# Optimization experiments

Measured on AMD Instinct MI355X. Metric: run time of the kernel, lower is better.

## Reference

```python
import jax, jax.numpy as jnp
import numpy as np
import math

B, L, D = 4, 2048, 1024        # batch, x_len, x_dim
QKV, H = 64, 16                # qkv_dim, head_dim (number of heads)


def setup_inputs() -> dict:
    key = jax.random.key(0)
    ks = jax.random.split(key, 10)
    s = 1.0 / math.sqrt(D)
    return {
        "x": jax.random.normal(ks[0], (B, L, D), jnp.float32),
        "encoder_x": jax.random.normal(ks[1], (B, L, D), jnp.float32),
        "Wq": jax.random.normal(ks[2], (D, QKV * H), jnp.float32) * s,
        "bq": jax.random.normal(ks[3], (QKV * H,), jnp.float32) * 0.01,
        "Wk": jax.random.normal(ks[4], (D, QKV * H), jnp.float32) * s,
        "bk": jax.random.normal(ks[5], (QKV * H,), jnp.float32) * 0.01,
        "Wv": jax.random.normal(ks[6], (D, QKV * H), jnp.float32) * s,
        "bv": jax.random.normal(ks[7], (QKV * H,), jnp.float32) * 0.01,
        "Wo": jax.random.normal(ks[8], (QKV * H, D), jnp.float32) * s,
        "bo": jax.random.normal(ks[9], (D,), jnp.float32) * 0.01,
    }


def reference(x, encoder_x, Wq, bq, Wk, bk, Wv, bv, Wo, bo):
    # q,k from encoder_x; v from x  -> [B, L, H, QKV]
    q = (encoder_x @ Wq + bq).reshape(B, L, H, QKV)
    k = (encoder_x @ Wk + bk).reshape(B, L, H, QKV)
    v = (x @ Wv + bv).reshape(B, L, H, QKV)
    # explicit [B,H,L,L] score matrix + softmax over k (faithful to source)
    scores = jax.nn.softmax(
        jnp.einsum("bqhd,bkhd->bhqk", q, k) / math.sqrt(QKV), axis=-1
    )
    # faithful to source einsum 'bvhd,bhqk->bvhd': no shared contraction
    # index, so scores are summed over (q,k) and broadcast onto v per (b,h).
    attn = jnp.einsum("bvhd,bhqk->bvhd", v, scores).reshape(B, L, H * QKV)
    return attn @ Wo + bo
```

## Files before the change

kernel.cpp:

```cpp
#include <hip/hip_runtime.h>
#include <stdint.h>


typedef __attribute__((ext_vector_type(8))) short bf16x8;
typedef __attribute__((ext_vector_type(4))) float f32x4;

typedef __attribute__((address_space(1))) void as1_void;
typedef __attribute__((address_space(3))) void as3_void;
#define GLD16(g, s)                                                          \
  __builtin_amdgcn_global_load_lds((as1_void*)(g), (as3_void*)(s), 16, 0, 0)

__device__ __forceinline__ short f2bf(float f) {
  union { float f; uint32_t u; } v; v.f = f;
  uint32_t r = v.u + 0x7FFFu + ((v.u >> 16) & 1u);
  return (short)(r >> 16);
}

__device__ __forceinline__ bf16x8 pack8(f32x4 a, f32x4 b) {
  union { f32x4 f; uint32_t u[4]; } x, y;
  x.f = a; y.f = b;
#pragma unroll
  for (int t = 0; t < 4; ++t) x.u[t] += 0x8000u;
#pragma unroll
  for (int t = 0; t < 4; ++t) y.u[t] += 0x8000u;
  union { bf16x8 v; uint32_t u[4]; } o;
  o.u[0] = __builtin_amdgcn_perm(x.u[1], x.u[0], 0x07060302);
  o.u[1] = __builtin_amdgcn_perm(x.u[3], x.u[2], 0x07060302);
  o.u[2] = __builtin_amdgcn_perm(y.u[1], y.u[0], 0x07060302);
  o.u[3] = __builtin_amdgcn_perm(y.u[3], y.u[2], 0x07060302);
  return o.v;
}

__global__ __launch_bounds__(256) void wgemm(
    const float* __restrict__ Wo, const float* __restrict__ Wv,
    const float* __restrict__ bv, const float* __restrict__ bo,
    short* __restrict__ Wt, float* __restrict__ biasc) {
  constexpr int BK = 64, NW = 1024;
  __shared__ __align__(16) float Bsf[64 * BK];
  __shared__ __align__(16) float Ts[64 * 36];
  const int b = blockIdx.x, tid = threadIdx.x;

  if (b >= 512) {
    float* red = Bsf;
    const int b3 = b - 512;
    const int nx = tid & 15, ky = tid >> 4;
    const int n = b3 * 16 + nx;
    float s = 0.f;
    for (int k = ky; k < 1024; k += 16)
      s += bv[k] * Wo[(size_t)k * NW + n];
    red[tid] = s;
    __syncthreads();
#pragma unroll
    for (int st = 128; st >= 16; st >>= 1) {
      if (tid < st) red[tid] += red[tid + st];
      __syncthreads();
    }
    if (ky == 0) biasc[n] = 2048.0f * red[nx] + bo[n];
    return;
  }

  const int lane = tid & 63, wave = tid >> 6;
  const int bm = (b >> 4) * 32, bn = (b & 15) * 64;
  const int wm = (wave & 1) * 16, wn = (wave >> 1) * 32;
  const int l15 = lane & 15, quad = lane >> 4;

  f32x4 acc[2];
  acc[0] = (f32x4){0.f, 0.f, 0.f, 0.f};
  acc[1] = (f32x4){0.f, 0.f, 0.f, 0.f};

  const int br = tid >> 4, bc4 = (tid & 15) ^ (br & 7);
  const float* pb = Wv + (size_t)(bn + br) * NW + bc4 * 4;
  float* lb = Bsf + tid * 4;

  const int ajr = tid >> 3, ac4 = (tid & 7) * 4;
  const float* pa = Wo + (size_t)ajr * NW + bm + ac4;

  for (int kt = 0; kt < 1024; kt += BK) {
    float4 va = *(const float4*)(pa);
    float4 vb = *(const float4*)(pa + 32 * (size_t)NW);
    pa += (size_t)BK * NW;
#pragma unroll
    for (int s = 0; s < 4; ++s) GLD16(pb + (size_t)(16 * s) * NW, lb + 1024 * s);
    pb += BK;
    *(float4*)(Ts + ajr * 36 + ac4) = va;
    *(float4*)(Ts + (ajr + 32) * 36 + ac4) = vb;
    __syncthreads();
#pragma unroll
    for (int kk = 0; kk < 2; ++kk) {
      const float* tsp = Ts + ((kk * 4 + quad) * 8) * 36 + wm + l15;
      float av[8];
#pragma unroll
      for (int e = 0; e < 8; ++e) av[e] = tsp[e * 36];
      bf16x8 af = pack8((f32x4){av[0], av[1], av[2], av[3]},
                        (f32x4){av[4], av[5], av[6], av[7]});
#pragma unroll
      for (int j = 0; j < 2; ++j) {
        const int rn = wn + j * 16 + l15;
        const int c4 = kk * 8 + quad * 2;
        f32x4 u0 = *(const f32x4*)(Bsf + (rn * 16 + (c4 ^ (rn & 7))) * 4);
        f32x4 u1 = *(const f32x4*)(Bsf + (rn * 16 + ((c4 + 1) ^ (rn & 7))) * 4);
        acc[j] = __builtin_amdgcn_mfma_f32_16x16x32_bf16(af, pack8(u0, u1),
                                                         acc[j], 0, 0, 0);
      }
    }
    __syncthreads();
  }
#pragma unroll
  for (int j = 0; j < 2; ++j) {
    const int col = bn + wn + j * 16 + l15;
    const int row0 = bm + wm + quad * 4;
#pragma unroll
    for (int r = 0; r < 4; ++r)
      Wt[(size_t)(row0 + r) * NW + col] = f2bf(2048.f * acc[j][r]);
  }
}

__global__ __launch_bounds__(256) void gemm_main(
    const float* __restrict__ X, const short* __restrict__ Bt,
    const float* __restrict__ bias, float* __restrict__ Out,
    int M, int N, int K) {
  constexpr int BK = 64;
  __shared__ __align__(16) char smem[65536];
  short* As0 = (short*)smem;
  short* As1 = (short*)(smem + 16384);
  short* Bs0 = (short*)(smem + 32768);
  short* Bs1 = (short*)(smem + 49152);
  const int tid = threadIdx.x, lane = tid & 63, wave = tid >> 6;
  const int b = blockIdx.x;
  const int bm = (b & 63) * 128;
  const int bn = (b >> 6) * 128;
  const int wm = (wave & 1) * 64, wn = (wave >> 1) * 64;
  const int l15 = lane & 15, quad = lane >> 4;

  f32x4 acc[4][4];
#pragma unroll
  for (int i = 0; i < 4; ++i)
#pragma unroll
    for (int j = 0; j < 4; ++j) acc[i][j] = (f32x4){0.f, 0.f, 0.f, 0.f};

  const int srow = tid >> 3, sc8 = (tid & 7) ^ (srow & 7);
  const float* pa = X + (size_t)(bm + srow) * K + sc8 * 8;
  const short* pb = Bt + (size_t)(bn + srow) * K + sc8 * 8;

  float4 a0[4], a1[4];

#define LOADA(kt)                                                            \
  {                                                                          \
    _Pragma("unroll") for (int s = 0; s < 4; ++s) {                          \
      const float* p = pa + (size_t)(32 * s) * K + (kt);                     \
      a0[s] = *(const float4*)(p);                                           \
      a1[s] = *(const float4*)(p + 4);                                       \
    }                                                                        \
  }
#define LOADB(Bsx, kt)                                                       \
  {                                                                          \
    _Pragma("unroll") for (int s = 0; s < 4; ++s)                            \
        GLD16(pb + (size_t)(32 * s) * K + (kt), (Bsx) + tid * 8 + 2048 * s); \
  }
#define PACKWRITE(Asx)                                                       \
  {                                                                          \
    _Pragma("unroll") for (int s = 0; s < 4; ++s)                            \
        *(bf16x8*)((Asx) + tid * 8 + 2048 * s) =                             \
            pack8((f32x4){a0[s].x, a0[s].y, a0[s].z, a0[s].w},               \
                  (f32x4){a1[s].x, a1[s].y, a1[s].z, a1[s].w});              \
  }
#define COMPUTE(Asx, Bsx)                                                    \
  {                                                                          \
    _Pragma("unroll") for (int kk = 0; kk < 2; ++kk) {                       \
      bf16x8 af[4], bfr[4];                                                  \
      _Pragma("unroll") for (int i = 0; i < 4; ++i) {                        \
        const int r = wm + i * 16 + l15;                                     \
        af[i] = *(const bf16x8*)((Asx) + r * BK +                            \
                                 ((kk * 4 + quad) ^ (r & 7)) * 8);           \
      }                                                                      \
      _Pragma("unroll") for (int j = 0; j < 4; ++j) {                        \
        const int r = wn + j * 16 + l15;                                     \
        bfr[j] = *(const bf16x8*)((Bsx) + r * BK +                           \
                                  ((kk * 4 + quad) ^ (r & 7)) * 8);          \
      }                                                                      \
      _Pragma("unroll") for (int i = 0; i < 4; ++i)                          \
          _Pragma("unroll") for (int j = 0; j < 4; ++j)                      \
              acc[i][j] = __builtin_amdgcn_mfma_f32_16x16x32_bf16(           \
                  af[i], bfr[j], acc[i][j], 0, 0, 0);                        \
    }                                                                        \
  }

  LOADA(0);
  LOADB(Bs0, 0);
  PACKWRITE(As0);
  __syncthreads();

  for (int trip = 0; trip < 8; ++trip) {
    const int kt_o = trip * 128 + 64;
    LOADA(kt_o);
    LOADB(Bs1, kt_o);
    COMPUTE(As0, Bs0);
    PACKWRITE(As1);
    __syncthreads();
    if (trip < 7) {
      const int kt_n = trip * 128 + 128;
      LOADA(kt_n);
      LOADB(Bs0, kt_n);
      COMPUTE(As1, Bs1);
      PACKWRITE(As0);
    } else {
      COMPUTE(As1, Bs1);
    }
    __syncthreads();
  }
#undef LOADA
#undef LOADB
#undef PACKWRITE
#undef COMPUTE

  float* T = (float*)smem + wave * 1088;
#pragma unroll
  for (int i = 0; i < 4; ++i) {
#pragma unroll
    for (int j = 0; j < 4; ++j) {
      const float bb = bias[bn + wn + j * 16 + l15];
#pragma unroll
      for (int r = 0; r < 4; ++r)
        T[(quad * 4 + r) * 68 + j * 16 + l15] = acc[i][j][r] + bb;
    }
#pragma unroll
    for (int p = 0; p < 4; ++p) {
      const int row = (lane >> 4) + 4 * p;
      const int ch = lane & 15;
      f32x4 v = *(const f32x4*)(T + row * 68 + ch * 4);
      *(f32x4*)(Out + (size_t)(bm + wm + i * 16 + row) * N + bn + wn +
                ch * 4) = v;
    }
  }
}

extern "C" void kernel_launch(void* const* d_in, const int* in_sizes, int n_in,
                              void* d_out, int out_size, void* d_ws,
                              size_t ws_size, hipStream_t stream) {
  const float* x  = (const float*)d_in[0];
  const float* Wv = (const float*)d_in[6];
  const float* bv = (const float*)d_in[7];
  const float* Wo = (const float*)d_in[8];
  const float* bo = (const float*)d_in[9];
  float* out = (float*)d_out;

  constexpr int D = 1024, NO = 1024;
  constexpr int M = 8192;

  char* ws = (char*)d_ws;
  short* wt_bf = (short*)(ws);
  float* biasc = (float*)(ws + (2u << 20));

  wgemm<<<576, 256, 0, stream>>>(Wo, Wv, bv, bo, wt_bf, biasc);
  gemm_main<<<(M / 128) * (NO / 128), 256, 0, stream>>>(
      x, wt_bf, biasc, out, M, NO, D);
}
```

Before: 166.9 us.

## Pre-convert x to bf16 and stream both GEMM operands via direct LDS loads

Adds a pass to the prep kernel that converts x from fp32 to bf16 into workspace, using extra blocks. The main GEMM then loads both A and B tiles asynchronously with global_load_lds, instead of loading fp32 A into registers and packing it into LDS. This removes the per-tile VALU conversion, the register staging and the doubled fp32 A traffic that is repeated across the N-tiles. In exchange it adds a standalone read of x plus a write of the bf16 copy, and it restructures the barrier placement in the double-buffered loop.

```diff
diff --git a/kernel.cpp b/kernel.cpp
--- a/kernel.cpp
+++ b/kernel.cpp
@@ -31,14 +31,24 @@
   return o.v;
 }
 
-__global__ __launch_bounds__(256) void wgemm(
+__global__ __launch_bounds__(256) void mid(
     const float* __restrict__ Wo, const float* __restrict__ Wv,
     const float* __restrict__ bv, const float* __restrict__ bo,
+    const float* __restrict__ x, short* __restrict__ x_bf,
     short* __restrict__ Wt, float* __restrict__ biasc) {
   constexpr int BK = 64, NW = 1024;
   __shared__ __align__(16) float Bsf[64 * BK];
   __shared__ __align__(16) float Ts[64 * 36];
   const int b = blockIdx.x, tid = threadIdx.x;
+
+  if (b >= 576) {
+    const int i = (b - 576) * 256 + tid;
+    const float4* p = (const float4*)x;
+    float4 a = p[2 * (size_t)i], c = p[2 * (size_t)i + 1];
+    *(bf16x8*)(x_bf + 8 * (size_t)i) =
+        pack8((f32x4){a.x, a.y, a.z, a.w}, (f32x4){c.x, c.y, c.z, c.w});
+    return;
+  }
 
   if (b >= 512) {
     float* red = Bsf;
@@ -116,14 +126,14 @@
 }
 
 __global__ __launch_bounds__(256) void gemm_main(
-    const float* __restrict__ X, const short* __restrict__ Bt,
+    const short* __restrict__ A, const short* __restrict__ Bt,
     const float* __restrict__ bias, float* __restrict__ Out,
     int M, int N, int K) {
   constexpr int BK = 64;
   __shared__ __align__(16) char smem[65536];
   short* As0 = (short*)smem;
-  short* As1 = (short*)(smem + 16384);
-  short* Bs0 = (short*)(smem + 32768);
+  short* Bs0 = (short*)(smem + 16384);
+  short* As1 = (short*)(smem + 32768);
   short* Bs1 = (short*)(smem + 49152);
   const int tid = threadIdx.x, lane = tid & 63, wave = tid >> 6;
   const int b = blockIdx.x;
@@ -139,30 +149,15 @@
     for (int j = 0; j < 4; ++j) acc[i][j] = (f32x4){0.f, 0.f, 0.f, 0.f};
 
   const int srow = tid >> 3, sc8 = (tid & 7) ^ (srow & 7);
-  const float* pa = X + (size_t)(bm + srow) * K + sc8 * 8;
+  const short* pa = A + (size_t)(bm + srow) * K + sc8 * 8;
   const short* pb = Bt + (size_t)(bn + srow) * K + sc8 * 8;
 
-  float4 a0[4], a1[4];
-
-#define LOADA(kt)                                                            \
-  {                                                                          \
-    _Pragma("unroll") for (int s = 0; s < 4; ++s) {                          \
-      const float* p = pa + (size_t)(32 * s) * K + (kt);                     \
-      a0[s] = *(const float4*)(p);                                           \
-      a1[s] = *(const float4*)(p + 4);                                       \
-    }                                                                        \
-  }
-#define LOADB(Bsx, kt)                                                       \
+#define STAGE(Asx, Bsx, kt)                                                  \
   {                                                                          \
     _Pragma("unroll") for (int s = 0; s < 4; ++s)                            \
+        GLD16(pa + (size_t)(32 * s) * K + (kt), (Asx) + tid * 8 + 2048 * s); \
+    _Pragma("unroll") for (int s = 0; s < 4; ++s)                            \
         GLD16(pb + (size_t)(32 * s) * K + (kt), (Bsx) + tid * 8 + 2048 * s); \
-  }
-#define PACKWRITE(Asx)                                                       \
-  {                                                                          \
-    _Pragma("unroll") for (int s = 0; s < 4; ++s)                            \
-        *(bf16x8*)((Asx) + tid * 8 + 2048 * s) =                             \
-            pack8((f32x4){a0[s].x, a0[s].y, a0[s].z, a0[s].w},               \
-                  (f32x4){a1[s].x, a1[s].y, a1[s].z, a1[s].w});              \
   }
 #define COMPUTE(Asx, Bsx)                                                    \
   {                                                                          \
@@ -185,32 +180,23 @@
     }                                                                        \
   }
 
-  LOADA(0);
-  LOADB(Bs0, 0);
-  PACKWRITE(As0);
+  STAGE(As0, Bs0, 0);
   __syncthreads();
 
   for (int trip = 0; trip < 8; ++trip) {
-    const int kt_o = trip * 128 + 64;
-    LOADA(kt_o);
-    LOADB(Bs1, kt_o);
+    const int kt_e = trip * 128;
+    STAGE(As1, Bs1, kt_e + 64);
     COMPUTE(As0, Bs0);
-    PACKWRITE(As1);
     __syncthreads();
     if (trip < 7) {
-      const int kt_n = trip * 128 + 128;
-      LOADA(kt_n);
-      LOADB(Bs0, kt_n);
+      STAGE(As0, Bs0, kt_e + 128);
       COMPUTE(As1, Bs1);
-      PACKWRITE(As0);
+      __syncthreads();
     } else {
       COMPUTE(As1, Bs1);
     }
-    __syncthreads();
-  }
-#undef LOADA
-#undef LOADB
-#undef PACKWRITE
+  }
+#undef STAGE
 #undef COMPUTE
 
   float* T = (float*)smem + wave * 1088;
@@ -248,10 +234,11 @@
   constexpr int M = 8192;
 
   char* ws = (char*)d_ws;
-  short* wt_bf = (short*)(ws);
-  float* biasc = (float*)(ws + (2u << 20));
-
-  wgemm<<<576, 256, 0, stream>>>(Wo, Wv, bv, bo, wt_bf, biasc);
+  short* x_bf  = (short*)(ws);
+  short* wt_bf = (short*)(ws + (16u << 20));
+  float* biasc = (float*)(ws + (18u << 20));
+
+  mid<<<4672, 256, 0, stream>>>(Wo, Wv, bv, bo, x, x_bf, wt_bf, biasc);
   gemm_main<<<(M / 128) * (NO / 128), 256, 0, stream>>>(
-      x, wt_bf, biasc, out, M, NO, D);
-}
+      x_bf, wt_bf, biasc, out, M, NO, D);
+}
```

Measured after the change: 153.9 us. 7.8% less time.
